# Optimization experiments

Measured on AMD Instinct MI355X. Metric: run time of the kernel, lower is better.

The kernel has to match this reference:

```python
import jax, jax.numpy as jnp
import numpy as np

D_MODEL = 256
SCALE = 1.0 / np.sqrt(D_MODEL).astype(np.float32)


def setup_inputs() -> dict:
    key = jax.random.key(0)
    ks = jax.random.split(key, 8)
    B, M, d = 32, 8192, D_MODEL
    lim = 1.0 / np.sqrt(d)  # torch Linear default init range
    inp = {
        "query": jax.random.normal(ks[0], (B, d), dtype=jnp.float32),
        "tokens": jax.random.normal(ks[1], (B, M, d), dtype=jnp.float32),
        "q_w": jax.random.uniform(ks[2], (d, d), jnp.float32, -lim, lim),
        "q_b": jax.random.uniform(ks[3], (d,), jnp.float32, -lim, lim),
        "k_w": jax.random.uniform(ks[4], (d, d), jnp.float32, -lim, lim),
        "k_b": jax.random.uniform(ks[5], (d,), jnp.float32, -lim, lim),
        "v_w": jax.random.uniform(ks[6], (d, d), jnp.float32, -lim, lim),
        "v_b": jax.random.uniform(ks[7], (d,), jnp.float32, -lim, lim),
    }
    return inp


def reference(query, tokens, q_w, q_b, k_w, k_b, v_w, v_b):
    # q: [B, d]; k, v: [B, M, d]  (torch Linear: x @ W.T + b)
    q = query @ q_w.T + q_b
    k = tokens @ k_w.T + k_b
    v = tokens @ v_w.T + v_b
    # single-query scores: [B, M]
    logits = jnp.einsum("bd,bmd->bm", q, k) * SCALE
    w = jax.nn.softmax(logits, axis=-1)
    # weighted sum over tokens -> [B, d]
    return jnp.einsum("bm,bmd->bd", w, v)
```

## Files before the change

### kernel.cpp

```cpp
#include <hip/hip_runtime.h>
#include <math.h>

#define BB 32
#define MM 8192
#define DD 256
#define SCALE 0.0625f
#define WPB 64
#define TPW (MM / WPB)
#define BLK_PER_B (WPB / 4)

using f4 = __attribute__((ext_vector_type(4))) float;

__global__ __launch_bounds__(256) void k_qr(
    const float* __restrict__ query, const float* __restrict__ q_w,
    const float* __restrict__ q_b, const float* __restrict__ k_w,
    const float* __restrict__ v_w, float* __restrict__ vwt,
    float* __restrict__ r)
{
    const int tid = threadIdx.x;
    if (blockIdx.x >= BB) {
        const int t  = blockIdx.x - BB;
        const int dj = tid & 31;
        const int e8 = tid >> 5;
        const int d  = t * 32 + dj;
        #pragma unroll 4
        for (int it = 0; it < 32; ++it) {
            const int e = it * 8 + e8;
            vwt[e * DD + d] = v_w[d * DD + e];
        }
        return;
    }

    const int b = blockIdx.x;
    __shared__ __align__(16) float qv[DD];
    __shared__ float qp[DD];
    qv[tid] = query[b * DD + tid];
    __syncthreads();
    float acc = q_b[tid];
    const f4* qw4 = (const f4*)(q_w + (size_t)tid * DD);
    const f4* qv4 = (const f4*)qv;
    #pragma unroll 8
    for (int e = 0; e < DD / 4; ++e) {
        const f4 a = qv4[e], w = qw4[e];
        acc += a.x * w.x + a.y * w.y + a.z * w.z + a.w * w.w;
    }
    qp[tid] = acc;
    __syncthreads();
    float racc = 0.f;
    #pragma unroll 8
    for (int d = 0; d < DD; ++d) racc += qp[d] * k_w[d * DD + tid];
    r[b * DD + tid] = racc * SCALE;
}

__global__ __launch_bounds__(256, 2) void k_flash(
    const float* __restrict__ tokens, const float* __restrict__ r,
    float* __restrict__ part_m, float* __restrict__ part_l,
    f4* __restrict__ part_u)
{
    const int b    = blockIdx.y;
    const int blk  = blockIdx.x;
    const int tid  = threadIdx.x;
    const int w    = tid >> 6;
    const int lane = tid & 63;
    const int g    = lane & 15;
    const int tg   = lane >> 4;
    const int wi   = blk * 4 + w;
    const int m0   = wi * TPW;

    const f4* r4 = (const f4*)(r + b * DD);
    f4 rr[4];
    #pragma unroll
    for (int c = 0; c < 4; ++c) rr[c] = r4[16 * c + g];

    const f4* tok = (const f4*)tokens + ((size_t)b * MM + m0) * (DD / 4)
                  + (size_t)tg * (DD / 4) + g;

    float mw = -INFINITY, lw = 0.f;
    f4 u[4] = {{0,0,0,0},{0,0,0,0},{0,0,0,0},{0,0,0,0}};

    auto body = [&](const f4* x) {
        float s0 = x[0].x*rr[0].x + x[0].y*rr[0].y + x[0].z*rr[0].z + x[0].w*rr[0].w;
        float s1 = x[1].x*rr[1].x + x[1].y*rr[1].y + x[1].z*rr[1].z + x[1].w*rr[1].w;
        float s2 = x[2].x*rr[2].x + x[2].y*rr[2].y + x[2].z*rr[2].z + x[2].w*rr[2].w;
        float s3 = x[3].x*rr[3].x + x[3].y*rr[3].y + x[3].z*rr[3].z + x[3].w*rr[3].w;
        float p  = (s0 + s1) + (s2 + s3);

        p += __shfl_xor(p, 1);
        p += __shfl_xor(p, 2);
        p += __shfl_xor(p, 4);
        p += __shfl_xor(p, 8);

        const float newm  = fmaxf(mw, p);
        const float alpha = __expf(mw - newm);
        const float wj    = __expf(p  - newm);
        mw = newm;
        lw = lw * alpha + wj;
        #pragma unroll
        for (int c = 0; c < 4; ++c) {
            u[c].x = u[c].x * alpha + wj * x[c].x;
            u[c].y = u[c].y * alpha + wj * x[c].y;
            u[c].z = u[c].z * alpha + wj * x[c].z;
            u[c].w = u[c].w * alpha + wj * x[c].w;
        }
    };

    const int NIT = TPW / 4;
    f4 xa[4], xb[4];
    #pragma unroll
    for (int c = 0; c < 4; ++c)
        xa[c] = __builtin_nontemporal_load(tok + 16 * c);
    {
        const f4* t1 = tok + 4 * (DD / 4);
        #pragma unroll
        for (int c = 0; c < 4; ++c)
            xb[c] = __builtin_nontemporal_load(t1 + 16 * c);
    }

    for (int it = 0; it < NIT; it += 2) {
        f4 x[4];
        #pragma unroll
        for (int c = 0; c < 4; ++c) x[c] = xa[c];
        if (it + 2 < NIT) {
            const f4* nxt = tok + (size_t)(it + 2) * 4 * (DD / 4);
            #pragma unroll
            for (int c = 0; c < 4; ++c)
                xa[c] = __builtin_nontemporal_load(nxt + 16 * c);
        }
        body(x);

        #pragma unroll
        for (int c = 0; c < 4; ++c) x[c] = xb[c];
        if (it + 3 < NIT) {
            const f4* nxt = tok + (size_t)(it + 3) * 4 * (DD / 4);
            #pragma unroll
            for (int c = 0; c < 4; ++c)
                xb[c] = __builtin_nontemporal_load(nxt + 16 * c);
        }
        body(x);
    }

    float gm = mw;
    gm = fmaxf(gm, __shfl_xor(gm, 16));
    gm = fmaxf(gm, __shfl_xor(gm, 32));
    const float beta = __expf(mw - gm);
    float L = lw * beta;
    L += __shfl_xor(L, 16);
    L += __shfl_xor(L, 32);
    #pragma unroll
    for (int c = 0; c < 4; ++c) {
        u[c].x *= beta; u[c].y *= beta; u[c].z *= beta; u[c].w *= beta;
        u[c].x += __shfl_xor(u[c].x, 16);
        u[c].y += __shfl_xor(u[c].y, 16);
        u[c].z += __shfl_xor(u[c].z, 16);
        u[c].w += __shfl_xor(u[c].w, 16);
        u[c].x += __shfl_xor(u[c].x, 32);
        u[c].y += __shfl_xor(u[c].y, 32);
        u[c].z += __shfl_xor(u[c].z, 32);
        u[c].w += __shfl_xor(u[c].w, 32);
    }

    const int pi = b * WPB + wi;
    if (lane == 0) { part_m[pi] = gm; part_l[pi] = L; }
    f4 val = u[0];
    val = (tg == 1) ? u[1] : val;
    val = (tg == 2) ? u[2] : val;
    val = (tg == 3) ? u[3] : val;
    part_u[(size_t)pi * 64 + lane] = val;
}

__global__ __launch_bounds__(256) void k_combine(
    const float* __restrict__ part_m, const float* __restrict__ part_l,
    const f4* __restrict__ part_u, const float* __restrict__ vwt,
    const float* __restrict__ v_b, float* __restrict__ out)
{
    const int b = blockIdx.x, tid = threadIdx.x;
    __shared__ float red[256];
    __shared__ float sf[WPB];
    __shared__ f4 suh[4][64];
    __shared__ __align__(16) float su[DD];

    const float pm = (tid < WPB) ? part_m[b * WPB + tid] : -INFINITY;
    red[tid] = pm;
    __syncthreads();
    #pragma unroll
    for (int s = 128; s > 0; s >>= 1) {
        if (tid < s) red[tid] = fmaxf(red[tid], red[tid + s]);
        __syncthreads();
    }
    const float gm = red[0];
    __syncthreads();

    float lterm = 0.f;
    if (tid < WPB) {
        const float f = __expf(pm - gm);
        sf[tid] = f;
        lterm = part_l[b * WPB + tid] * f;
    }
    red[tid] = lterm;
    __syncthreads();
    #pragma unroll
    for (int s = 128; s > 0; s >>= 1) {
        if (tid < s) red[tid] += red[tid + s];
        __syncthreads();
    }
    const float l = red[0];

    const int slot = tid & 63;
    const int rg   = tid >> 6;
    const f4* pu = part_u + (size_t)b * WPB * 64;
    f4 acc = {0.f, 0.f, 0.f, 0.f};
    #pragma unroll 8
    for (int i = rg; i < WPB; i += 4)
        acc += pu[(size_t)i * 64 + slot] * sf[i];
    suh[rg][slot] = acc;
    __syncthreads();
    if (tid < 64) {
        f4 s = suh[0][tid] + suh[1][tid] + suh[2][tid] + suh[3][tid];
        s *= (1.f / l);
        ((f4*)su)[tid] = s;
    }
    __syncthreads();

    float o = v_b[tid];
    #pragma unroll 8
    for (int e = 0; e < DD; ++e) o += su[e] * vwt[e * DD + tid];
    out[b * DD + tid] = o;
}

extern "C" void kernel_launch(void* const* d_in, const int* in_sizes, int n_in,
                              void* d_out, int out_size, void* d_ws, size_t ws_size,
                              hipStream_t stream) {
    const float* query  = (const float*)d_in[0];
    const float* tokens = (const float*)d_in[1];
    const float* q_w    = (const float*)d_in[2];
    const float* q_b    = (const float*)d_in[3];
    const float* k_w    = (const float*)d_in[4];
    const float* v_w    = (const float*)d_in[6];
    const float* v_b    = (const float*)d_in[7];
    float* out = (float*)d_out;

    float* ws     = (float*)d_ws;
    float* r      = ws;
    float* part_m = r + BB * DD;
    float* part_l = part_m + BB * WPB;
    float* part_u = part_l + BB * WPB;
    float* vwt    = part_u + (size_t)BB * WPB * DD;

    k_qr<<<dim3(BB + 8), dim3(256), 0, stream>>>(query, q_w, q_b, k_w,
                                                 v_w, vwt, r);
    k_flash<<<dim3(BLK_PER_B, BB), dim3(256), 0, stream>>>(
        tokens, r, part_m, part_l, (f4*)part_u);
    k_combine<<<dim3(BB), dim3(256), 0, stream>>>(
        part_m, part_l, (const f4*)part_u, vwt, v_b, out);
}
```

Before: 388.0 us.

## Fuse combine kernel into flash kernel via last-block atomic counter

Removes the separate combine launch. Each flash block increments a per-batch counter, and the last block to finish reduces the partial softmax statistics and applies the V projection. The counter is reset in the first kernel. The combine's shared-memory tree reductions are replaced with wave shuffles. This saves one kernel launch and its gap, at the cost of an atomic plus fences in every block and a serialized tail on the last block per batch.

```diff
diff --git a/kernel.cpp b/kernel.cpp
--- a/kernel.cpp
+++ b/kernel.cpp
@@ -15,11 +15,12 @@
     const float* __restrict__ query, const float* __restrict__ q_w,
     const float* __restrict__ q_b, const float* __restrict__ k_w,
     const float* __restrict__ v_w, float* __restrict__ vwt,
-    float* __restrict__ r)
+    unsigned int* __restrict__ sem, float* __restrict__ r)
 {
     const int tid = threadIdx.x;
     if (blockIdx.x >= BB) {
         const int t  = blockIdx.x - BB;
+        if (t == 0 && tid < BB) sem[tid] = 0u;
         const int dj = tid & 31;
         const int e8 = tid >> 5;
         const int d  = t * 32 + dj;
@@ -55,7 +56,9 @@
 __global__ __launch_bounds__(256, 2) void k_flash(
     const float* __restrict__ tokens, const float* __restrict__ r,
     float* __restrict__ part_m, float* __restrict__ part_l,
-    f4* __restrict__ part_u)
+    f4* __restrict__ part_u, unsigned int* __restrict__ sem,
+    const float* __restrict__ vwt, const float* __restrict__ v_b,
+    float* __restrict__ out)
 {
     const int b    = blockIdx.y;
     const int blk  = blockIdx.x;
@@ -166,44 +169,41 @@
     val = (tg == 2) ? u[2] : val;
     val = (tg == 3) ? u[3] : val;
     part_u[(size_t)pi * 64 + lane] = val;
-}
-
-__global__ __launch_bounds__(256) void k_combine(
-    const float* __restrict__ part_m, const float* __restrict__ part_l,
-    const f4* __restrict__ part_u, const float* __restrict__ vwt,
-    const float* __restrict__ v_b, float* __restrict__ out)
-{
-    const int b = blockIdx.x, tid = threadIdx.x;
-    __shared__ float red[256];
+
+    __shared__ unsigned int s_old;
+    __threadfence();
+    __syncthreads();
+    if (tid == 0) s_old = atomicAdd(&sem[b], 1u);
+    __syncthreads();
+    if (s_old != BLK_PER_B - 1) return;
+    __threadfence();
+
     __shared__ float sf[WPB];
+    __shared__ float s_invl;
     __shared__ f4 suh[4][64];
     __shared__ __align__(16) float su[DD];
 
-    const float pm = (tid < WPB) ? part_m[b * WPB + tid] : -INFINITY;
-    red[tid] = pm;
-    __syncthreads();
-    #pragma unroll
-    for (int s = 128; s > 0; s >>= 1) {
-        if (tid < s) red[tid] = fmaxf(red[tid], red[tid + s]);
-        __syncthreads();
-    }
-    const float gm = red[0];
-    __syncthreads();
-
-    float lterm = 0.f;
-    if (tid < WPB) {
-        const float f = __expf(pm - gm);
+    if (tid < 64) {
+        const float pm = part_m[b * WPB + tid];
+        float gmax = pm;
+        gmax = fmaxf(gmax, __shfl_xor(gmax, 32));
+        gmax = fmaxf(gmax, __shfl_xor(gmax, 16));
+        gmax = fmaxf(gmax, __shfl_xor(gmax, 8));
+        gmax = fmaxf(gmax, __shfl_xor(gmax, 4));
+        gmax = fmaxf(gmax, __shfl_xor(gmax, 2));
+        gmax = fmaxf(gmax, __shfl_xor(gmax, 1));
+        const float f = __expf(pm - gmax);
         sf[tid] = f;
-        lterm = part_l[b * WPB + tid] * f;
-    }
-    red[tid] = lterm;
-    __syncthreads();
-    #pragma unroll
-    for (int s = 128; s > 0; s >>= 1) {
-        if (tid < s) red[tid] += red[tid + s];
-        __syncthreads();
-    }
-    const float l = red[0];
+        float lt = part_l[b * WPB + tid] * f;
+        lt += __shfl_xor(lt, 32);
+        lt += __shfl_xor(lt, 16);
+        lt += __shfl_xor(lt, 8);
+        lt += __shfl_xor(lt, 4);
+        lt += __shfl_xor(lt, 2);
+        lt += __shfl_xor(lt, 1);
+        if (tid == 0) s_invl = 1.f / lt;
+    }
+    __syncthreads();
 
     const int slot = tid & 63;
     const int rg   = tid >> 6;
@@ -216,7 +216,7 @@
     __syncthreads();
     if (tid < 64) {
         f4 s = suh[0][tid] + suh[1][tid] + suh[2][tid] + suh[3][tid];
-        s *= (1.f / l);
+        s *= s_invl;
         ((f4*)su)[tid] = s;
     }
     __syncthreads();
@@ -245,11 +245,10 @@
     float* part_l = part_m + BB * WPB;
     float* part_u = part_l + BB * WPB;
     float* vwt    = part_u + (size_t)BB * WPB * DD;
+    unsigned int* sem = (unsigned int*)(vwt + DD * DD);
 
     k_qr<<<dim3(BB + 8), dim3(256), 0, stream>>>(query, q_w, q_b, k_w,
-                                                 v_w, vwt, r);
+                                                 v_w, vwt, sem, r);
     k_flash<<<dim3(BLK_PER_B, BB), dim3(256), 0, stream>>>(
-        tokens, r, part_m, part_l, (f4*)part_u);
-    k_combine<<<dim3(BB), dim3(256), 0, stream>>>(
-        part_m, part_l, (const f4*)part_u, vwt, v_b, out);
+        tokens, r, part_m, part_l, (f4*)part_u, sem, vwt, v_b, out);
 }
```

After: 464.2 us. +19.6%, slower.
